# Optimization experiments

Measured on AMD Instinct MI355X. Metric: run time of the kernel, lower is better.

The kernel has to match this reference:

```python
import jax, jax.numpy as jnp
import numpy as np

N = 100000
E = 1600000
IN_C = 128
OUT_C = 64  # hidden_channels * 2


def setup_inputs() -> dict:
    key = jax.random.key(0)
    k1, k2, k3, k4 = jax.random.split(key, 4)
    x = jax.random.normal(k1, (N, IN_C), dtype=jnp.float32)
    edge_index = jax.random.randint(k2, (2, E), 0, N, dtype=jnp.int64)
    # GCNConv linear weight (stored as [in, out]; equivalent to PyG's lin.weight.T)
    std = 1.0 / np.sqrt(OUT_C)
    weight = jax.random.uniform(k3, (IN_C, OUT_C), dtype=jnp.float32, minval=-std, maxval=std)
    bias = jax.random.uniform(k4, (OUT_C,), dtype=jnp.float32, minval=-std, maxval=std)
    return {"x": x, "edge_index": edge_index, "weight": weight, "bias": bias}


def reference(x, edge_index, weight, bias):
    n = x.shape[0]
    # add self-loops (PyG GCNConv default)
    loops = jnp.arange(n, dtype=edge_index.dtype)
    src = jnp.concatenate([edge_index[0], loops])  # message sources (j)
    dst = jnp.concatenate([edge_index[1], loops])  # aggregation targets (i)

    xw = x @ weight  # [N, OUT_C]

    # symmetric normalization: deg over targets incl. self-loops
    deg = jax.ops.segment_sum(jnp.ones_like(dst, dtype=x.dtype), dst, num_segments=n)
    dinv = jnp.where(deg > 0, jax.lax.rsqrt(deg), 0.0)
    norm = dinv[src] * dinv[dst]  # [E+N]

    msg = xw[src] * norm[:, None]  # gather + scale: [E+N, OUT_C]
    out = jax.ops.segment_sum(msg, dst, num_segments=n)  # scatter-add
    return out + bias
```

## Files before the change

### kernel.cpp

```cpp
#include <hip/hip_runtime.h>
#include <stdint.h>

#define CAP 64
#define CAP_SHIFT 6
#define NSLICE 8
#define SUBSZ 196
#define B_E 4096
#define SCAP 1024
#define PAIR1_CAP (220*1024)
#define B2 2048
#define BPS2 128
#define SCAP2 96
#define PAIR2_CAP 3840

typedef int vint4 __attribute__((ext_vector_type(4)));
typedef float vfloat2 __attribute__((ext_vector_type(2)));
typedef float vf32x4 __attribute__((ext_vector_type(4)));
typedef short vs8 __attribute__((ext_vector_type(8)));

__device__ __forceinline__ unsigned short f2bf(float f) {
    union { float f; unsigned u; } v; v.f = f;
    unsigned r = v.u + 0x7FFF + ((v.u >> 16) & 1);
    return (unsigned short)(r >> 16);
}
__device__ __forceinline__ float bf2f(unsigned short h) {
    union { unsigned u; float f; } v; v.u = ((unsigned)h) << 16;
    return v.f;
}
__device__ __forceinline__ float bflo(unsigned u) {
    union { unsigned u; float f; } v; v.u = u << 16; return v.f;
}
__device__ __forceinline__ float bfhi(unsigned u) {
    union { unsigned u; float f; } v; v.u = u & 0xFFFF0000u; return v.f;
}

__global__ __launch_bounds__(256) void k_part(const int* __restrict__ eidx, int E,
                                              int slice_sz,
                                              unsigned* __restrict__ pairs1,
                                              int* __restrict__ cursor1) {
    __shared__ unsigned buf[NSLICE][SCAP];
    __shared__ int lcnt[NSLICE];
    __shared__ int lbase[NSLICE];
    int t = threadIdx.x;
    if (t < NSLICE) lcnt[t] = 0;
    __syncthreads();

    int base = blockIdx.x * B_E;
    int rem = E - base; if (rem > B_E) rem = B_E;

    auto ins = [&](int s, int d) {
        int sl = (unsigned)d / (unsigned)slice_sz;
        unsigned w = ((unsigned)(d - sl * slice_sz) << 17) | (unsigned)s;
        int p = atomicAdd(&lcnt[sl], 1);
        if (p < SCAP) buf[sl][p] = w;
        else {
            int gp = atomicAdd(&cursor1[sl], 1);
            if (gp < PAIR1_CAP) pairs1[(size_t)sl * PAIR1_CAP + gp] = w;
        }
    };

    int nvec = rem >> 2;
    const vint4* s4p = (const vint4*)(eidx + base);
    const vint4* d4p = (const vint4*)(eidx + E + base);
    for (int v = t; v < nvec; v += 256) {
        vint4 s4 = __builtin_nontemporal_load(s4p + v);
        vint4 d4 = __builtin_nontemporal_load(d4p + v);
        ins(s4.x, d4.x); ins(s4.y, d4.y); ins(s4.z, d4.z); ins(s4.w, d4.w);
    }
    for (int e = (nvec << 2) + t; e < rem; e += 256)
        ins(eidx[base + e], eidx[E + base + e]);

    __syncthreads();
    if (t < NSLICE) {
        int c = lcnt[t]; if (c > SCAP) c = SCAP;
        lcnt[t] = c;
        lbase[t] = (c > 0) ? atomicAdd(&cursor1[t], c) : 0;
    }
    __syncthreads();
    for (int sl = 0; sl < NSLICE; ++sl) {
        int c = lcnt[sl];
        unsigned* dst = pairs1 + (size_t)sl * PAIR1_CAP + lbase[sl];
        for (int j = t; j < c; j += 256)
            if (lbase[sl] + j < PAIR1_CAP) dst[j] = buf[sl][j];
    }
}

__global__ __launch_bounds__(256) void k_part2(const unsigned* __restrict__ pairs1,
                                               const int* __restrict__ cursor1,
                                               unsigned* __restrict__ pairs2,
                                               int* __restrict__ cursor2, int nsub) {
    __shared__ unsigned buf[64][SCAP2];
    __shared__ int lcnt[64];
    __shared__ int lbase[64];
    int slice = blockIdx.x & (NSLICE - 1);
    int bid   = blockIdx.x >> 3;
    int t = threadIdx.x;
    if (t < 64) lcnt[t] = 0;
    __syncthreads();

    int len = cursor1[slice]; if (len > PAIR1_CAP) len = PAIR1_CAP;
    int start = bid * B2;
    int end = start + B2; if (end > len) end = len;
    const unsigned* p = pairs1 + (size_t)slice * PAIR1_CAP;
    int cbase = slice * nsub;

    for (int j = start + t; j < end; j += 256) {
        unsigned e = p[j];
        int dl = e >> 17;
        int sub = (unsigned)dl / SUBSZ;
        unsigned w = ((unsigned)(dl - sub * SUBSZ) << 17) | (e & 0x1FFFFu);
        int pos = atomicAdd(&lcnt[sub], 1);
        if (pos < SCAP2) buf[sub][pos] = w;
        else {
            int gp = atomicAdd(&cursor2[cbase + sub], 1);
            if (gp < PAIR2_CAP) pairs2[(size_t)(cbase + sub) * PAIR2_CAP + gp] = w;
        }
    }
    __syncthreads();
    if (t < 64) {
        int c = lcnt[t]; if (c > SCAP2) c = SCAP2;
        lcnt[t] = c;
        lbase[t] = (c > 0) ? atomicAdd(&cursor2[cbase + t], c) : 0;
    }
    __syncthreads();
    for (int sub = 0; sub < 64; ++sub) {
        int c = lcnt[sub];
        if (c == 0) continue;
        unsigned* dst = pairs2 + (size_t)(cbase + sub) * PAIR2_CAP + lbase[sub];
        for (int j = t; j < c; j += 256)
            if (lbase[sub] + j < PAIR2_CAP) dst[j] = buf[sub][j];
    }
}

__global__ __launch_bounds__(256) void k_csr(const unsigned* __restrict__ pairs2,
                                             const int* __restrict__ cursor2,
                                             int* __restrict__ cnt,
                                             int* __restrict__ col,
                                             int nsub, int slice_sz, int n) {
    __shared__ int lcol[SUBSZ * CAP];
    __shared__ int lcnt[SUBSZ];
    int b = blockIdx.x;
    int slice = b / nsub, sub = b % nsub;
    int node_base = slice * slice_sz + sub * SUBSZ;
    int slice_hi = (slice + 1) * slice_sz; if (slice_hi > n) slice_hi = n;
    int nn = slice_hi - node_base; if (nn > SUBSZ) nn = SUBSZ;
    int t = threadIdx.x;
    if (t < SUBSZ) lcnt[t] = 0;
    __syncthreads();

    int len = cursor2[b]; if (len > PAIR2_CAP) len = PAIR2_CAP;
    const unsigned* p = pairs2 + (size_t)b * PAIR2_CAP;
    for (int j = t; j < len; j += 256) {
        unsigned e = p[j];
        int dsub = e >> 17;
        int s = (int)(e & 0x1FFFFu);
        int pos = atomicAdd(&lcnt[dsub], 1);
        if (pos < CAP) lcol[(dsub << CAP_SHIFT) + pos] = s;
    }
    __syncthreads();
    if (nn > 0) {
        vint4* cdst = (vint4*)(col + ((size_t)node_base << CAP_SHIFT));
        const vint4* csrc = (const vint4*)lcol;
        int m = nn * 16;
        for (int j = t; j < m; j += 256)
            __builtin_nontemporal_store(csrc[j], cdst + j);
        for (int j = t; j < nn; j += 256)
            cnt[node_base + j] = lcnt[j];
    }
}

__global__ __launch_bounds__(256) void k_gemm(const float* __restrict__ x,
                                              const float* __restrict__ w,
                                              const int* __restrict__ cnt,
                                              unsigned short* __restrict__ xwh, int n) {
    __shared__ unsigned short wT[64 * 128];
    int t = threadIdx.x;
    int row0 = blockIdx.x * 64;

    {
        int c = t & 63;
        int kg = t >> 6;
        const float* wp = w + c;
#pragma unroll
        for (int k2 = 0; k2 < 32; k2 += 2) {
            int k = kg * 32 + k2;
            float f0 = wp[(size_t)k * 64];
            float f1 = wp[(size_t)(k + 1) * 64];
            unsigned pk = (unsigned)f2bf(f0) | ((unsigned)f2bf(f1) << 16);
            int bo = (c * 256 + k * 2) ^ ((c & 7) << 4);
            *(unsigned*)((char*)wT + bo) = pk;
        }
    }
    __syncthreads();

    int lane = t & 63;
    int wid = t >> 6;
    int lr = lane & 15;
    int lg = lane >> 4;
    int rbase = row0 + wid * 16;
    int grow = rbase + lr;
    int gr = grow < n ? grow : 0;
    const float* xr = x + (size_t)gr * 128 + lg * 8;

    vf32x4 acc0 = {0.f,0.f,0.f,0.f}, acc1 = {0.f,0.f,0.f,0.f};
    vf32x4 acc2 = {0.f,0.f,0.f,0.f}, acc3 = {0.f,0.f,0.f,0.f};
#pragma unroll
    for (int ks = 0; ks < 4; ++ks) {
        float4 v0 = *(const float4*)(xr + ks * 32);
        float4 v1 = *(const float4*)(xr + ks * 32 + 4);
        vs8 a;
        a[0] = (short)f2bf(v0.x); a[1] = (short)f2bf(v0.y);
        a[2] = (short)f2bf(v0.z); a[3] = (short)f2bf(v0.w);
        a[4] = (short)f2bf(v1.x); a[5] = (short)f2bf(v1.y);
        a[6] = (short)f2bf(v1.z); a[7] = (short)f2bf(v1.w);
        int kb = (ks * 32 + lg * 8) * 2;
        int c0 = lr,      o0 = (c0 * 256 + kb) ^ ((c0 & 7) << 4);
        int c1 = 16 + lr, o1 = (c1 * 256 + kb) ^ ((c1 & 7) << 4);
        int c2 = 32 + lr, o2 = (c2 * 256 + kb) ^ ((c2 & 7) << 4);
        int c3 = 48 + lr, o3 = (c3 * 256 + kb) ^ ((c3 & 7) << 4);
        vs8 b0 = *(const vs8*)((char*)wT + o0);
        vs8 b1 = *(const vs8*)((char*)wT + o1);
        vs8 b2 = *(const vs8*)((char*)wT + o2);
        vs8 b3 = *(const vs8*)((char*)wT + o3);
        acc0 = __builtin_amdgcn_mfma_f32_16x16x32_bf16(a, b0, acc0, 0, 0, 0);
        acc1 = __builtin_amdgcn_mfma_f32_16x16x32_bf16(a, b1, acc1, 0, 0, 0);
        acc2 = __builtin_amdgcn_mfma_f32_16x16x32_bf16(a, b2, acc2, 0, 0, 0);
        acc3 = __builtin_amdgcn_mfma_f32_16x16x32_bf16(a, b3, acc3, 0, 0, 0);
    }

    int srow = rbase + lg * 4;
    float dv[4];
#pragma unroll
    for (int r = 0; r < 4; ++r) {
        int row = srow + r;
        int cc = (row < n) ? cnt[row] : 0;
        dv[r] = rsqrtf((float)cc + 1.0f);
    }
#pragma unroll
    for (int r = 0; r < 4; ++r) {
        int row = srow + r;
        if (row < n) {
            unsigned short* op = xwh + (size_t)row * 64 + lr;
            op[0]  = f2bf(acc0[r] * dv[r]);
            op[16] = f2bf(acc1[r] * dv[r]);
            op[32] = f2bf(acc2[r] * dv[r]);
            op[48] = f2bf(acc3[r] * dv[r]);
        }
    }
}

__global__ __launch_bounds__(256) void k_agg(const int* __restrict__ cnt,
                                             const int* __restrict__ col,
                                             const unsigned short* __restrict__ xwh,
                                             const float* __restrict__ bias,
                                             float* __restrict__ out, int n) {
    int lane = threadIdx.x & 63;
    int wid = __builtin_amdgcn_readfirstlane(threadIdx.x >> 6);
    int i = blockIdx.x * 4 + wid;
    if (i >= n) return;
    int c = lane & 31;
    int half = lane >> 5;
    const unsigned* xw32 = (const unsigned*)xwh;

    int dr = cnt[i];
    float di = rsqrtf((float)dr + 1.0f);
    int deg = dr > CAP ? CAP : dr;
    int colv = 0;
    if (lane < deg) colv = col[(i << CAP_SHIFT) + lane];
    unsigned su = xw32[(i << 5) + c];
    vfloat2 bv = *(const vfloat2*)(bias + 2 * c);

    float a0 = 0.f, a1 = 0.f;
    int k = 0;
    for (; k + 16 <= deg; k += 16) {
        int j0 = __shfl(colv, k + 0  + half, 64);
        int j1 = __shfl(colv, k + 2  + half, 64);
        int j2 = __shfl(colv, k + 4  + half, 64);
        int j3 = __shfl(colv, k + 6  + half, 64);
        int j4 = __shfl(colv, k + 8  + half, 64);
        int j5 = __shfl(colv, k + 10 + half, 64);
        int j6 = __shfl(colv, k + 12 + half, 64);
        int j7 = __shfl(colv, k + 14 + half, 64);
        unsigned u0 = xw32[(j0 << 5) + c];
        unsigned u1 = xw32[(j1 << 5) + c];
        unsigned u2 = xw32[(j2 << 5) + c];
        unsigned u3 = xw32[(j3 << 5) + c];
        unsigned u4 = xw32[(j4 << 5) + c];
        unsigned u5 = xw32[(j5 << 5) + c];
        unsigned u6 = xw32[(j6 << 5) + c];
        unsigned u7 = xw32[(j7 << 5) + c];
        a0 += bflo(u0); a1 += bfhi(u0);
        a0 += bflo(u1); a1 += bfhi(u1);
        a0 += bflo(u2); a1 += bfhi(u2);
        a0 += bflo(u3); a1 += bfhi(u3);
        a0 += bflo(u4); a1 += bfhi(u4);
        a0 += bflo(u5); a1 += bfhi(u5);
        a0 += bflo(u6); a1 += bfhi(u6);
        a0 += bflo(u7); a1 += bfhi(u7);
    }
    for (; k + 8 <= deg; k += 8) {
        int j0 = __shfl(colv, k + 0 + half, 64);
        int j1 = __shfl(colv, k + 2 + half, 64);
        int j2 = __shfl(colv, k + 4 + half, 64);
        int j3 = __shfl(colv, k + 6 + half, 64);
        unsigned u0 = xw32[(j0 << 5) + c];
        unsigned u1 = xw32[(j1 << 5) + c];
        unsigned u2 = xw32[(j2 << 5) + c];
        unsigned u3 = xw32[(j3 << 5) + c];
        a0 += bflo(u0); a1 += bfhi(u0);
        a0 += bflo(u1); a1 += bfhi(u1);
        a0 += bflo(u2); a1 += bfhi(u2);
        a0 += bflo(u3); a1 += bfhi(u3);
    }
    for (; k + 4 <= deg; k += 4) {
        int j0 = __shfl(colv, k + 0 + half, 64);
        int j1 = __shfl(colv, k + 2 + half, 64);
        unsigned u0 = xw32[(j0 << 5) + c];
        unsigned u1 = xw32[(j1 << 5) + c];
        a0 += bflo(u0); a1 += bfhi(u0);
        a0 += bflo(u1); a1 += bfhi(u1);
    }
    {
        int idx0 = k + half;
        int s0 = idx0 < 64 ? idx0 : 0;
        int j0 = __shfl(colv, s0, 64);
        if (idx0 < deg) {
            unsigned u = xw32[(j0 << 5) + c];
            a0 += bflo(u); a1 += bfhi(u);
        }
        int idx1 = k + 2 + half;
        int s1 = idx1 < 64 ? idx1 : 0;
        int j1 = __shfl(colv, s1, 64);
        if (idx1 < deg) {
            unsigned u = xw32[(j1 << 5) + c];
            a0 += bflo(u); a1 += bfhi(u);
        }
    }
    a0 += __shfl_xor(a0, 32, 64);
    a1 += __shfl_xor(a1, 32, 64);
    a0 += bflo(su); a1 += bfhi(su);
    if (half == 0) {
        vfloat2 o;
        o.x = fmaf(a0, di, bv.x);
        o.y = fmaf(a1, di, bv.y);
        __builtin_nontemporal_store(o, (vfloat2*)(out + ((long long)i << 6) + 2 * c));
    }
}

extern "C" void kernel_launch(void* const* d_in, const int* in_sizes, int n_in,
                              void* d_out, int out_size, void* d_ws, size_t ws_size,
                              hipStream_t stream) {
    const float* x    = (const float*)d_in[0];
    const int* eidx   = (const int*)d_in[1];
    const float* w    = (const float*)d_in[2];
    const float* bias = (const float*)d_in[3];
    float* out        = (float*)d_out;

    int out_c = in_sizes[3];
    int in_c  = in_sizes[2] / out_c;
    int n     = in_sizes[0] / in_c;
    int E     = in_sizes[1] / 2;

    int slice_sz = (n + NSLICE - 1) / NSLICE;
    int nsub = (slice_sz + SUBSZ - 1) / SUBSZ;

    char* ws = (char*)d_ws;
    int*      col     = (int*)ws;
    unsigned* pairs1  = (unsigned*)ws;
    size_t offA = (size_t)n * CAP * 4;
    int*      cnt     = (int*)(ws + offA);
    int*      cursor1 = (int*)(ws + offA + (size_t)n * 4);
    int*      cursor2 = cursor1 + NSLICE;
    char*     ubaseB  = ws + offA + (size_t)n * 4 + 4096;
    unsigned* pairs2  = (unsigned*)ubaseB;
    unsigned short* xwh = (unsigned short*)ubaseB;

    (void)hipMemsetAsync(cursor1, 0, (size_t)(NSLICE + NSLICE * nsub) * 4, stream);
    k_part <<<(E + B_E - 1) / B_E, 256, 0, stream>>>(eidx, E, slice_sz, pairs1, cursor1);
    k_part2<<<NSLICE * BPS2, 256, 0, stream>>>(pairs1, cursor1, pairs2, cursor2, nsub);
    k_csr  <<<NSLICE * nsub, 256, 0, stream>>>(pairs2, cursor2, cnt, col, nsub, slice_sz, n);
    k_gemm <<<(n + 63) / 64, 256, 0, stream>>>(x, w, cnt, xwh, n);
    k_agg  <<<(n + 3) / 4, 256, 0, stream>>>(cnt, col, xwh, bias, out, n);
}
```

Measured before the change: 187.3 us.

## Replace multi-pass partitioned CSR build with single global-atomic scatter kernel

Removes the two-level LDS radix partition (k_part, k_part2) and local CSR kernel, replacing them with one kernel that atomically increments per-node counts in global memory and writes source indices directly into the fixed-capacity column array. This eliminates two kernel launches and the intermediate pair buffers' write/read traffic. In exchange it issues one global atomic per edge and scattered, uncoalesced column writes, relying on cache to absorb them.

```diff
diff --git a/kernel.cpp b/kernel.cpp
--- a/kernel.cpp
+++ b/kernel.cpp
@@ -3,15 +3,6 @@
 
 #define CAP 64
 #define CAP_SHIFT 6
-#define NSLICE 8
-#define SUBSZ 196
-#define B_E 4096
-#define SCAP 1024
-#define PAIR1_CAP (220*1024)
-#define B2 2048
-#define BPS2 128
-#define SCAP2 96
-#define PAIR2_CAP 3840
 
 typedef int vint4 __attribute__((ext_vector_type(4)));
 typedef float vfloat2 __attribute__((ext_vector_type(2)));
@@ -34,138 +25,31 @@
     union { unsigned u; float f; } v; v.u = u & 0xFFFF0000u; return v.f;
 }
 
-__global__ __launch_bounds__(256) void k_part(const int* __restrict__ eidx, int E,
-                                              int slice_sz,
-                                              unsigned* __restrict__ pairs1,
-                                              int* __restrict__ cursor1) {
-    __shared__ unsigned buf[NSLICE][SCAP];
-    __shared__ int lcnt[NSLICE];
-    __shared__ int lbase[NSLICE];
-    int t = threadIdx.x;
-    if (t < NSLICE) lcnt[t] = 0;
-    __syncthreads();
-
-    int base = blockIdx.x * B_E;
-    int rem = E - base; if (rem > B_E) rem = B_E;
-
-    auto ins = [&](int s, int d) {
-        int sl = (unsigned)d / (unsigned)slice_sz;
-        unsigned w = ((unsigned)(d - sl * slice_sz) << 17) | (unsigned)s;
-        int p = atomicAdd(&lcnt[sl], 1);
-        if (p < SCAP) buf[sl][p] = w;
-        else {
-            int gp = atomicAdd(&cursor1[sl], 1);
-            if (gp < PAIR1_CAP) pairs1[(size_t)sl * PAIR1_CAP + gp] = w;
-        }
-    };
-
-    int nvec = rem >> 2;
-    const vint4* s4p = (const vint4*)(eidx + base);
-    const vint4* d4p = (const vint4*)(eidx + E + base);
-    for (int v = t; v < nvec; v += 256) {
-        vint4 s4 = __builtin_nontemporal_load(s4p + v);
-        vint4 d4 = __builtin_nontemporal_load(d4p + v);
-        ins(s4.x, d4.x); ins(s4.y, d4.y); ins(s4.z, d4.z); ins(s4.w, d4.w);
-    }
-    for (int e = (nvec << 2) + t; e < rem; e += 256)
-        ins(eidx[base + e], eidx[E + base + e]);
-
-    __syncthreads();
-    if (t < NSLICE) {
-        int c = lcnt[t]; if (c > SCAP) c = SCAP;
-        lcnt[t] = c;
-        lbase[t] = (c > 0) ? atomicAdd(&cursor1[t], c) : 0;
-    }
-    __syncthreads();
-    for (int sl = 0; sl < NSLICE; ++sl) {
-        int c = lcnt[sl];
-        unsigned* dst = pairs1 + (size_t)sl * PAIR1_CAP + lbase[sl];
-        for (int j = t; j < c; j += 256)
-            if (lbase[sl] + j < PAIR1_CAP) dst[j] = buf[sl][j];
-    }
-}
-
-__global__ __launch_bounds__(256) void k_part2(const unsigned* __restrict__ pairs1,
-                                               const int* __restrict__ cursor1,
-                                               unsigned* __restrict__ pairs2,
-                                               int* __restrict__ cursor2, int nsub) {
-    __shared__ unsigned buf[64][SCAP2];
-    __shared__ int lcnt[64];
-    __shared__ int lbase[64];
-    int slice = blockIdx.x & (NSLICE - 1);
-    int bid   = blockIdx.x >> 3;
-    int t = threadIdx.x;
-    if (t < 64) lcnt[t] = 0;
-    __syncthreads();
-
-    int len = cursor1[slice]; if (len > PAIR1_CAP) len = PAIR1_CAP;
-    int start = bid * B2;
-    int end = start + B2; if (end > len) end = len;
-    const unsigned* p = pairs1 + (size_t)slice * PAIR1_CAP;
-    int cbase = slice * nsub;
-
-    for (int j = start + t; j < end; j += 256) {
-        unsigned e = p[j];
-        int dl = e >> 17;
-        int sub = (unsigned)dl / SUBSZ;
-        unsigned w = ((unsigned)(dl - sub * SUBSZ) << 17) | (e & 0x1FFFFu);
-        int pos = atomicAdd(&lcnt[sub], 1);
-        if (pos < SCAP2) buf[sub][pos] = w;
-        else {
-            int gp = atomicAdd(&cursor2[cbase + sub], 1);
-            if (gp < PAIR2_CAP) pairs2[(size_t)(cbase + sub) * PAIR2_CAP + gp] = w;
-        }
-    }
-    __syncthreads();
-    if (t < 64) {
-        int c = lcnt[t]; if (c > SCAP2) c = SCAP2;
-        lcnt[t] = c;
-        lbase[t] = (c > 0) ? atomicAdd(&cursor2[cbase + t], c) : 0;
-    }
-    __syncthreads();
-    for (int sub = 0; sub < 64; ++sub) {
-        int c = lcnt[sub];
-        if (c == 0) continue;
-        unsigned* dst = pairs2 + (size_t)(cbase + sub) * PAIR2_CAP + lbase[sub];
-        for (int j = t; j < c; j += 256)
-            if (lbase[sub] + j < PAIR2_CAP) dst[j] = buf[sub][j];
-    }
-}
-
-__global__ __launch_bounds__(256) void k_csr(const unsigned* __restrict__ pairs2,
-                                             const int* __restrict__ cursor2,
-                                             int* __restrict__ cnt,
-                                             int* __restrict__ col,
-                                             int nsub, int slice_sz, int n) {
-    __shared__ int lcol[SUBSZ * CAP];
-    __shared__ int lcnt[SUBSZ];
-    int b = blockIdx.x;
-    int slice = b / nsub, sub = b % nsub;
-    int node_base = slice * slice_sz + sub * SUBSZ;
-    int slice_hi = (slice + 1) * slice_sz; if (slice_hi > n) slice_hi = n;
-    int nn = slice_hi - node_base; if (nn > SUBSZ) nn = SUBSZ;
-    int t = threadIdx.x;
-    if (t < SUBSZ) lcnt[t] = 0;
-    __syncthreads();
-
-    int len = cursor2[b]; if (len > PAIR2_CAP) len = PAIR2_CAP;
-    const unsigned* p = pairs2 + (size_t)b * PAIR2_CAP;
-    for (int j = t; j < len; j += 256) {
-        unsigned e = p[j];
-        int dsub = e >> 17;
-        int s = (int)(e & 0x1FFFFu);
-        int pos = atomicAdd(&lcnt[dsub], 1);
-        if (pos < CAP) lcol[(dsub << CAP_SHIFT) + pos] = s;
-    }
-    __syncthreads();
-    if (nn > 0) {
-        vint4* cdst = (vint4*)(col + ((size_t)node_base << CAP_SHIFT));
-        const vint4* csrc = (const vint4*)lcol;
-        int m = nn * 16;
-        for (int j = t; j < m; j += 256)
-            __builtin_nontemporal_store(csrc[j], cdst + j);
-        for (int j = t; j < nn; j += 256)
-            cnt[node_base + j] = lcnt[j];
+__global__ __launch_bounds__(256) void k_build(const int* __restrict__ eidx, int E,
+                                               int* __restrict__ cnt,
+                                               int* __restrict__ col) {
+    int t = blockIdx.x * 256 + threadIdx.x;
+    int nvec = E >> 2;
+    const vint4* s4p = (const vint4*)eidx;
+    const vint4* d4p = (const vint4*)(eidx + E);
+    if (t < nvec) {
+        vint4 s4 = __builtin_nontemporal_load(s4p + t);
+        vint4 d4 = __builtin_nontemporal_load(d4p + t);
+        int p0 = atomicAdd(&cnt[d4.x], 1);
+        int p1 = atomicAdd(&cnt[d4.y], 1);
+        int p2 = atomicAdd(&cnt[d4.z], 1);
+        int p3 = atomicAdd(&cnt[d4.w], 1);
+        if (p0 < CAP) col[(d4.x << CAP_SHIFT) + p0] = s4.x;
+        if (p1 < CAP) col[(d4.y << CAP_SHIFT) + p1] = s4.y;
+        if (p2 < CAP) col[(d4.z << CAP_SHIFT) + p2] = s4.z;
+        if (p3 < CAP) col[(d4.w << CAP_SHIFT) + p3] = s4.w;
+    }
+    if (t < (E & 3)) {
+        int e = (nvec << 2) + t;
+        int s = eidx[e];
+        int d = eidx[E + e];
+        int p = atomicAdd(&cnt[d], 1);
+        if (p < CAP) col[(d << CAP_SHIFT) + p] = s;
     }
 }
 
@@ -361,24 +245,15 @@
     int n     = in_sizes[0] / in_c;
     int E     = in_sizes[1] / 2;
 
-    int slice_sz = (n + NSLICE - 1) / NSLICE;
-    int nsub = (slice_sz + SUBSZ - 1) / SUBSZ;
-
     char* ws = (char*)d_ws;
-    int*      col     = (int*)ws;
-    unsigned* pairs1  = (unsigned*)ws;
+    int*      col = (int*)ws;
     size_t offA = (size_t)n * CAP * 4;
-    int*      cnt     = (int*)(ws + offA);
-    int*      cursor1 = (int*)(ws + offA + (size_t)n * 4);
-    int*      cursor2 = cursor1 + NSLICE;
-    char*     ubaseB  = ws + offA + (size_t)n * 4 + 4096;
-    unsigned* pairs2  = (unsigned*)ubaseB;
-    unsigned short* xwh = (unsigned short*)ubaseB;
-
-    (void)hipMemsetAsync(cursor1, 0, (size_t)(NSLICE + NSLICE * nsub) * 4, stream);
-    k_part <<<(E + B_E - 1) / B_E, 256, 0, stream>>>(eidx, E, slice_sz, pairs1, cursor1);
-    k_part2<<<NSLICE * BPS2, 256, 0, stream>>>(pairs1, cursor1, pairs2, cursor2, nsub);
-    k_csr  <<<NSLICE * nsub, 256, 0, stream>>>(pairs2, cursor2, cnt, col, nsub, slice_sz, n);
+    int*      cnt = (int*)(ws + offA);
+    unsigned short* xwh = (unsigned short*)(ws + offA + (size_t)n * 4 + 4096);
+
+    (void)hipMemsetAsync(cnt, 0, (size_t)n * 4, stream);
+    int nvec = E >> 2;
+    k_build<<<(nvec + 255) / 256, 256, 0, stream>>>(eidx, E, cnt, col);
     k_gemm <<<(n + 63) / 64, 256, 0, stream>>>(x, w, cnt, xwh, n);
     k_agg  <<<(n + 3) / 4, 256, 0, stream>>>(cnt, col, xwh, bias, out, n);
 }
```

After: 273.1 us. +45.8%, slower.
